# Optimization experiments

Measured on AMD Instinct MI355X. Metric: run time of the kernel, lower is better.

The kernel has to match this reference:

```python
import jax, jax.numpy as jnp
import numpy as np

N, E, D, L1 = 100000, 1600000, 128, 64


def setup_inputs() -> dict:
    key = jax.random.key(0)
    ks = jax.random.split(key, 8)
    return {
        "x": jax.random.normal(ks[0], (N, D), dtype=jnp.float32),
        "edge_index": jax.random.randint(ks[1], (2, E), 0, N, dtype=jnp.int64),
        "W1_rel": jax.random.normal(ks[2], (L1, D), dtype=jnp.float32) * (1.0 / np.sqrt(D)),
        "b1": jax.random.normal(ks[3], (L1,), dtype=jnp.float32) * 0.01,
        "W1_root": jax.random.normal(ks[4], (L1, D), dtype=jnp.float32) * (1.0 / np.sqrt(D)),
        "W2_rel": jax.random.normal(ks[5], (1, L1), dtype=jnp.float32) * (1.0 / np.sqrt(L1)),
        "b2": jax.random.normal(ks[6], (1,), dtype=jnp.float32) * 0.01,
        "W2_root": jax.random.normal(ks[7], (1, L1), dtype=jnp.float32) * (1.0 / np.sqrt(L1)),
    }


def _graph_conv(h, src, dst, W_rel, b, W_root, n):
    # PyG GraphConv: lin_rel(sum_{j in N(i)} h_j) + lin_root(h_i)
    agg = jax.ops.segment_sum(h[src], dst, num_segments=n)  # [N, d_in]
    return agg @ W_rel.T + b + h @ W_root.T


def reference(x, edge_index, W1_rel, b1, W1_root, W2_rel, b2, W2_root):
    src, dst = edge_index[0], edge_index[1]
    n = x.shape[0]
    h = _graph_conv(x, src, dst, W1_rel, b1, W1_root, n)        # [N, L1]
    h = jax.nn.leaky_relu(h, negative_slope=0.2)                # dropout is identity in eval
    gate = _graph_conv(h, src, dst, W2_rel, b2, W2_root, n)     # [N, 1]
    gate = jax.nn.softmax(gate, axis=0)                         # softmax over nodes
    out = gate.T @ x                                            # [1, D]
    return out
```

## Files before the change

kernel.cpp:

```cpp
#include <hip/hip_runtime.h>
#include <cstdint>

#define DD 128
#define LL 64
#define PSTRIDE 64
#define NCHUNK 256
#define BPAD 784

typedef short short8 __attribute__((ext_vector_type(8)));
typedef float f32x4 __attribute__((ext_vector_type(4)));

static __device__ __forceinline__ unsigned short f2bf(float f) {
    unsigned u = __float_as_uint(f);
    unsigned r = (u + 0x7FFFu + ((u >> 16) & 1u)) >> 16;
    return (unsigned short)r;
}
static __device__ __forceinline__ float bf2f(unsigned short h) {
    return __uint_as_float(((unsigned)h) << 16);
}
static __device__ __forceinline__ uint4 pack8(float4 lo, float4 hi) {
    uint4 u;
    u.x = (unsigned)f2bf(lo.x) | ((unsigned)f2bf(lo.y) << 16);
    u.y = (unsigned)f2bf(lo.z) | ((unsigned)f2bf(lo.w) << 16);
    u.z = (unsigned)f2bf(hi.x) | ((unsigned)f2bf(hi.y) << 16);
    u.w = (unsigned)f2bf(hi.z) | ((unsigned)f2bf(hi.w) << 16);
    return u;
}

__global__ __launch_bounds__(256) void k1_scat(const float* __restrict__ x,
        const float* __restrict__ Wrel, const float* __restrict__ Wroot,
        const int* __restrict__ dst, int* __restrict__ cm,
        unsigned short* __restrict__ yb, unsigned short* __restrict__ zb,
        int n, int E)
{
    __shared__ __align__(16) unsigned short xa[64 * 128];
    int tid = threadIdx.x;
    if (blockIdx.x < NCHUNK) {
        int* hist = (int*)xa;
        int c = blockIdx.x;
        for (int i = tid; i < BPAD; i += 256) hist[i] = 0;
        __syncthreads();
        int CH = (E + NCHUNK - 1) / NCHUNK;
        int base = c * CH, end = base + CH; if (end > E) end = E;
        for (int e = base + tid; e < end; e += 256)
            atomicAdd(&hist[dst[e] >> 7], 1);
        __syncthreads();
        for (int i = tid; i < BPAD; i += 256) cm[c * BPAD + i] = hist[i];
        return;
    }
    int nbase = (blockIdx.x - NCHUNK) * 64;

    {
        int r = tid & 63, cb = (tid >> 6) * 4;
        int node = nbase + r; if (node >= n) node = n - 1;
        const float4* xp = (const float4*)(x + (size_t)node * DD + cb * 8);
        #pragma unroll
        for (int c = 0; c < 4; ++c) {
            float4 lo = xp[c * 2], hi = xp[c * 2 + 1];
            int slot = (cb + c + r) & 15;
            *(uint4*)&xa[r * 128 + slot * 8] = pack8(lo, hi);
        }
    }
    __syncthreads();

    int lane = tid & 63;
    int w = __builtin_amdgcn_readfirstlane(tid >> 6);
    int lr = lane & 15, lk = lane >> 4;
    const float* __restrict__ Wsel = (w < 2) ? Wrel : Wroot;
    int rbase = (w & 1) * 32;

    f32x4 acc[4][2];
    #pragma unroll
    for (int tr = 0; tr < 4; ++tr)
        #pragma unroll
        for (int tc = 0; tc < 2; ++tc)
            acc[tr][tc] = (f32x4){0.f, 0.f, 0.f, 0.f};

    #pragma unroll
    for (int kk = 0; kk < 4; ++kk) {
        int c = kk * 4 + lk;
        short8 bfrag[2];
        #pragma unroll
        for (int tc = 0; tc < 2; ++tc) {
            const float* wp = Wsel + (size_t)(rbase + tc * 16 + lr) * DD + kk * 32 + lk * 8;
            float4 lo = *(const float4*)wp;
            float4 hi = *(const float4*)(wp + 4);
            uint4 u = pack8(lo, hi);
            bfrag[tc] = *(short8*)&u;
        }
        #pragma unroll
        for (int tr = 0; tr < 4; ++tr) {
            int arow = tr * 16 + lr;
            short8 afrag = *(const short8*)&xa[arow * 128 + ((c + arow) & 15) * 8];
            acc[tr][0] = __builtin_amdgcn_mfma_f32_16x16x32_bf16(afrag, bfrag[0], acc[tr][0], 0, 0, 0);
            acc[tr][1] = __builtin_amdgcn_mfma_f32_16x16x32_bf16(afrag, bfrag[1], acc[tr][1], 0, 0, 0);
        }
    }

    __syncthreads();
    unsigned short* ob = xa;
    #pragma unroll
    for (int tr = 0; tr < 4; ++tr) {
        #pragma unroll
        for (int tc = 0; tc < 2; ++tc) {
            int col = w * 32 + tc * 16 + lr;
            int cg = col >> 4, ci = col & 15;
            #pragma unroll
            for (int r = 0; r < 4; ++r) {
                int row = tr * 16 + lk * 4 + r;
                ob[row * 128 + ((cg ^ (row & 7)) << 4) + ci] = f2bf(acc[tr][tc][r]);
            }
        }
    }
    __syncthreads();

    {
        int row = tid >> 2, part = tid & 3;
        int node = nbase + row;
        if (node < n) {
            int by = row * 128 + ((part ^ (row & 7)) << 4);
            uint4 a0 = *(uint4*)&ob[by];
            uint4 a1 = *(uint4*)&ob[by + 8];
            *(uint4*)(yb + (size_t)node * LL + part * 16) = a0;
            *(uint4*)(yb + (size_t)node * LL + part * 16 + 8) = a1;
            int bz = row * 128 + (((part + 4) ^ (row & 7)) << 4);
            uint4 b0 = *(uint4*)&ob[bz];
            uint4 b1 = *(uint4*)&ob[bz + 8];
            *(uint4*)(zb + (size_t)node * LL + part * 16) = b0;
            *(uint4*)(zb + (size_t)node * LL + part * 16 + 8) = b1;
        }
    }
}

__global__ __launch_bounds__(1024) void kB(int* __restrict__ cm, int* __restrict__ bbase, int E) {
    __shared__ int sc[1024];
    int b = threadIdx.x;
    int tot = 0;
    if (b < BPAD)
        for (int c = 0; c < NCHUNK; ++c) tot += cm[c * BPAD + b];
    sc[b] = tot;
    __syncthreads();
    for (int off = 1; off < 1024; off <<= 1) {
        int add = (b >= off) ? sc[b - off] : 0;
        __syncthreads();
        sc[b] += add;
        __syncthreads();
    }
    int excl = sc[b] - tot;
    if (b < BPAD) bbase[b] = excl;
    if (b == 1023) bbase[BPAD] = sc[b];
    if (b < BPAD) {
        int run = excl;
        for (int c = 0; c < NCHUNK; ++c) {
            int v = cm[c * BPAD + b];
            cm[c * BPAD + b] = run;
            run += v;
        }
    }
}

__global__ __launch_bounds__(256) void kC(const int* __restrict__ src, const int* __restrict__ dst,
        const int* __restrict__ cm, int* __restrict__ sorted, int E)
{
    __shared__ int run[BPAD];
    int c = blockIdx.x;
    for (int i = threadIdx.x; i < BPAD; i += 256) run[i] = cm[c * BPAD + i];
    __syncthreads();
    int CH = (E + NCHUNK - 1) / NCHUNK;
    int base = c * CH, end = base + CH; if (end > E) end = E;
    for (int e = base + threadIdx.x; e < end; e += 256) {
        int d = dst[e];
        int pos = atomicAdd(&run[d >> 7], 1);
        sorted[pos] = ((d & 127) << 17) | src[e];
    }
}

__global__ __launch_bounds__(256) void kD(const int* __restrict__ sorted, const int* __restrict__ bbase,
        int* __restrict__ cnt, int* __restrict__ csr_pad, int n)
{
    __shared__ int hist[128];
    int b = blockIdx.x;
    int lo = bbase[b], hi = bbase[b + 1];
    for (int i = threadIdx.x; i < 128; i += 256) hist[i] = 0;
    __syncthreads();
    for (int e = lo + threadIdx.x; e < hi; e += 256) {
        int v = sorted[e];
        int loc = v >> 17;
        int pos = atomicAdd(&hist[loc], 1);
        if (pos < PSTRIDE)
            csr_pad[(size_t)(b * 128 + loc) * PSTRIDE + pos] = v & 0x1FFFF;
    }
    __syncthreads();
    for (int i = threadIdx.x; i < 128; i += 256) {
        int node = b * 128 + i;
        if (node < n) cnt[node] = hist[i];
    }
}

__global__ __launch_bounds__(256) void k3_agg(const unsigned short* __restrict__ yb, const unsigned short* __restrict__ zb,
        const int* __restrict__ cnt, const int* __restrict__ csr_pad,
        const float* __restrict__ b1, const float* __restrict__ w2rel, const float* __restrict__ w2root,
        float* __restrict__ s, float* __restrict__ t, int n)
{
    int wave = threadIdx.x >> 6, lane = threadIdx.x & 63;
    int i = blockIdx.x * 4 + wave;
    if (i >= n) return;
    int deg = cnt[i]; if (deg > PSTRIDE) deg = PSTRIDE;
    const int* cp = csr_pad + (size_t)i * PSTRIDE;
    int c2 = lane & 31, half = lane >> 5;
    float ax = 0.f, ay = 0.f;
    int k = 0;
    for (; k + 4 <= deg; k += 4) {
        int sA0 = cp[k], sB0 = cp[k + 1], sA1 = cp[k + 2], sB1 = cp[k + 3];
        int r0 = half ? sB0 : sA0;
        int r1 = half ? sB1 : sA1;
        unsigned u0 = *(const unsigned*)(yb + (size_t)r0 * LL + c2 * 2);
        unsigned u1 = *(const unsigned*)(yb + (size_t)r1 * LL + c2 * 2);
        ax += bf2f((unsigned short)u0) + bf2f((unsigned short)u1);
        ay += bf2f((unsigned short)(u0 >> 16)) + bf2f((unsigned short)(u1 >> 16));
    }
    if (k + 2 <= deg) {
        int rA = cp[k], rB = cp[k + 1];
        int r = half ? rB : rA;
        unsigned u = *(const unsigned*)(yb + (size_t)r * LL + c2 * 2);
        ax += bf2f((unsigned short)u);
        ay += bf2f((unsigned short)(u >> 16));
        k += 2;
    }
    if (k < deg && !half) {
        int r = cp[k];
        unsigned u = *(const unsigned*)(yb + (size_t)r * LL + c2 * 2);
        ax += bf2f((unsigned short)u);
        ay += bf2f((unsigned short)(u >> 16));
    }
    ax += __shfl_xor(ax, 32, 64);
    ay += __shfl_xor(ay, 32, 64);

    unsigned uz = *(const unsigned*)(zb + (size_t)i * LL + c2 * 2);
    float hx = ax + bf2f((unsigned short)uz) + b1[c2 * 2];
    float hy = ay + bf2f((unsigned short)(uz >> 16)) + b1[c2 * 2 + 1];
    hx = hx > 0.f ? hx : 0.2f * hx;
    hy = hy > 0.f ? hy : 0.2f * hy;
    float sv = hx * w2rel[c2 * 2] + hy * w2rel[c2 * 2 + 1];
    float tv = hx * w2root[c2 * 2] + hy * w2root[c2 * 2 + 1];
    #pragma unroll
    for (int o = 16; o >= 1; o >>= 1) {
        sv += __shfl_xor(sv, o, 64);
        tv += __shfl_xor(tv, o, 64);
    }
    if (lane == 0) { s[i] = sv; t[i] = tv; }
}

static __device__ __forceinline__ void smcomb(float& m, float& Z, float m2, float Z2) {
    float M = fmaxf(m, m2);
    Z = Z * expf(m - M) + Z2 * expf(m2 - M);
    m = M;
}

__global__ __launch_bounds__(256) void k5_gate(const float* __restrict__ s, const float* __restrict__ t,
        const int* __restrict__ cnt, const int* __restrict__ csr_pad, const float* __restrict__ b2,
        float* __restrict__ g, float2* __restrict__ pairs, int n)
{
    __shared__ float sm[256], sz[256];
    int i = blockIdx.x * 256 + threadIdx.x;
    float m = -3.402823466e38f, Z = 0.f;
    if (i < n) {
        float acc = b2[0] + t[i];
        int deg = cnt[i]; if (deg > PSTRIDE) deg = PSTRIDE;
        const int* cp = csr_pad + (size_t)i * PSTRIDE;
        int e = 0;
        for (; e + 4 <= deg; e += 4)
            acc += (s[cp[e]] + s[cp[e + 1]]) + (s[cp[e + 2]] + s[cp[e + 3]]);
        for (; e < deg; ++e) acc += s[cp[e]];
        g[i] = acc;
        m = acc; Z = 1.f;
    }
    sm[threadIdx.x] = m; sz[threadIdx.x] = Z;
    __syncthreads();
    for (int off = 128; off > 0; off >>= 1) {
        if (threadIdx.x < off) {
            float mm = sm[threadIdx.x], ZZ = sz[threadIdx.x];
            smcomb(mm, ZZ, sm[threadIdx.x + off], sz[threadIdx.x + off]);
            sm[threadIdx.x] = mm; sz[threadIdx.x] = ZZ;
        }
        __syncthreads();
    }
    if (threadIdx.x == 0) pairs[blockIdx.x] = make_float2(sm[0], sz[0]);
}

__global__ __launch_bounds__(256) void k6b(const float2* __restrict__ pairs, float* __restrict__ scalars, int nb) {
    __shared__ float sm[256], sz[256];
    float m = -3.402823466e38f, Z = 0.f;
    for (int j = threadIdx.x; j < nb; j += 256) {
        float2 p = pairs[j];
        smcomb(m, Z, p.x, p.y);
    }
    sm[threadIdx.x] = m; sz[threadIdx.x] = Z;
    __syncthreads();
    for (int off = 128; off > 0; off >>= 1) {
        if (threadIdx.x < off) {
            float mm = sm[threadIdx.x], ZZ = sz[threadIdx.x];
            smcomb(mm, ZZ, sm[threadIdx.x + off], sz[threadIdx.x + off]);
            sm[threadIdx.x] = mm; sz[threadIdx.x] = ZZ;
        }
        __syncthreads();
    }
    if (threadIdx.x == 0) { scalars[0] = sm[0]; scalars[1] = sz[0]; }
}

__global__ __launch_bounds__(256) void k6_out(const float* __restrict__ x, const float* __restrict__ g,
        const float* __restrict__ scalars, float* __restrict__ out, int n)
{
    __shared__ float acc_s[4][DD];
    int wave = threadIdx.x >> 6, lane = threadIdx.x & 63;
    float m = scalars[0];
    float invZ = 1.0f / scalars[1];
    float a0 = 0.f, a1 = 0.f;
    int gw = blockIdx.x * 4 + wave;
    int nw = gridDim.x * 4;
    for (int i = gw; i < n; i += nw) {
        float w = expf(g[i] - m) * invZ;
        a0 += w * x[(size_t)i * DD + lane];
        a1 += w * x[(size_t)i * DD + 64 + lane];
    }
    acc_s[wave][lane] = a0;
    acc_s[wave][lane + 64] = a1;
    __syncthreads();
    if (wave == 0) {
        float v0 = acc_s[0][lane] + acc_s[1][lane] + acc_s[2][lane] + acc_s[3][lane];
        float v1 = acc_s[0][lane + 64] + acc_s[1][lane + 64] + acc_s[2][lane + 64] + acc_s[3][lane + 64];
        atomicAdd(&out[lane], v0);
        atomicAdd(&out[lane + 64], v1);
    }
}

extern "C" void kernel_launch(void* const* d_in, const int* in_sizes, int n_in,
                              void* d_out, int out_size, void* d_ws, size_t ws_size,
                              hipStream_t stream)
{
    const float* x      = (const float*)d_in[0];
    const int*   eidx   = (const int*)d_in[1];
    const float* W1rel  = (const float*)d_in[2];
    const float* b1     = (const float*)d_in[3];
    const float* W1root = (const float*)d_in[4];
    const float* W2rel  = (const float*)d_in[5];
    const float* b2     = (const float*)d_in[6];
    const float* W2root = (const float*)d_in[7];
    float* out = (float*)d_out;

    int n = in_sizes[0] / DD;
    int E = in_sizes[1] / 2;
    const int* src = eidx;
    const int* dstp = eidx + E;
    int NBK = (n + 127) >> 7;

    char* ws = (char*)d_ws;
    size_t off = 0;
    auto alloc = [&](size_t bytes) -> char* {
        char* p = ws + off;
        off = (off + bytes + 255) & ~(size_t)255;
        return p;
    };
    unsigned short* yb = (unsigned short*)alloc((size_t)n * LL * 2);
    unsigned short* zb = (unsigned short*)alloc((size_t)n * LL * 2);
    int*   cnt     = (int*)  alloc((size_t)n * 4);
    int*   csr_pad = (int*)  alloc((size_t)NBK * 128 * PSTRIDE * 4);
    int*   cm      = (int*)  alloc((size_t)NCHUNK * BPAD * 4);
    int*   bbase   = (int*)  alloc((size_t)(BPAD + 1) * 4);
    int*   sorted  = (int*)  alloc((size_t)E * 4);
    float* s       = (float*)alloc((size_t)n * 4);
    float* t       = (float*)alloc((size_t)n * 4);
    float* g       = (float*)alloc((size_t)n * 4);
    int ngate = (n + 255) / 256;
    float2* pairs  = (float2*)alloc((size_t)ngate * 8);
    float* scalars = (float*)alloc(2 * 4);
    (void)ws_size; (void)n_in;

    hipMemsetAsync(d_out, 0, (size_t)out_size * 4, stream);

    int nblk1 = (n + 63) / 64;
    k1_scat<<<NCHUNK + nblk1, 256, 0, stream>>>(x, W1rel, W1root, dstp, cm, yb, zb, n, E);
    kB<<<1, 1024, 0, stream>>>(cm, bbase, E);
    kC<<<NCHUNK, 256, 0, stream>>>(src, dstp, cm, sorted, E);
    kD<<<NBK, 256, 0, stream>>>(sorted, bbase, cnt, csr_pad, n);
    k3_agg<<<(n + 3) / 4, 256, 0, stream>>>(yb, zb, cnt, csr_pad, b1, W2rel, W2root, s, t, n);
    k5_gate<<<ngate, 256, 0, stream>>>(s, t, cnt, csr_pad, b2, g, pairs, n);
    k6b<<<1, 256, 0, stream>>>(pairs, scalars, ngate);
    k6_out<<<512, 256, 0, stream>>>(x, g, scalars, out, n);
}
```

Before: 203.8 us.

## Split bucket scan, coalesce x staging, unroll aggregation gather deeper

The single-block scan kernel, which walked the whole chunk-by-bucket count matrix twice with 784 threads, becomes two kernels. One does per-bucket running sums across 4 blocks, and a tiny kernel scans the bucket totals, with kC adding the bucket base when it loads its offsets. The x staging load in k1 now assigns four threads per row, so neighbouring threads read contiguous memory. The k3 gather loop is unrolled from 4 to 8 edges per iteration to keep more loads in flight, and the bf16 unpack of the high half uses a mask instead of a shift. This adds one extra kernel launch in exchange.

```diff
diff --git a/kernel.cpp b/kernel.cpp
--- a/kernel.cpp
+++ b/kernel.cpp
@@ -15,8 +15,11 @@
     unsigned r = (u + 0x7FFFu + ((u >> 16) & 1u)) >> 16;
     return (unsigned short)r;
 }
-static __device__ __forceinline__ float bf2f(unsigned short h) {
-    return __uint_as_float(((unsigned)h) << 16);
+static __device__ __forceinline__ float bflo(unsigned u) {
+    return __uint_as_float(u << 16);
+}
+static __device__ __forceinline__ float bfhi(unsigned u) {
+    return __uint_as_float(u & 0xFFFF0000u);
 }
 static __device__ __forceinline__ uint4 pack8(float4 lo, float4 hi) {
     uint4 u;
@@ -51,12 +54,12 @@
     int nbase = (blockIdx.x - NCHUNK) * 64;
 
     {
-        int r = tid & 63, cb = (tid >> 6) * 4;
+        int r = tid >> 2, cb = (tid & 3) * 4;
         int node = nbase + r; if (node >= n) node = n - 1;
-        const float4* xp = (const float4*)(x + (size_t)node * DD + cb * 8);
+        const float4* xp = (const float4*)(x + (size_t)node * DD);
         #pragma unroll
         for (int c = 0; c < 4; ++c) {
-            float4 lo = xp[c * 2], hi = xp[c * 2 + 1];
+            float4 lo = xp[(cb + c) * 2], hi = xp[(cb + c) * 2 + 1];
             int slot = (cb + c + r) & 15;
             *(uint4*)&xa[r * 128 + slot * 8] = pack8(lo, hi);
         }
@@ -132,13 +135,23 @@
     }
 }
 
-__global__ __launch_bounds__(1024) void kB(int* __restrict__ cm, int* __restrict__ bbase, int E) {
+__global__ __launch_bounds__(256) void kB1(int* __restrict__ cm, int* __restrict__ btot) {
+    int b = blockIdx.x * 256 + threadIdx.x;
+    if (b >= BPAD) return;
+    int run = 0;
+    for (int c = 0; c < NCHUNK; ++c) {
+        int v = cm[c * BPAD + b];
+        cm[c * BPAD + b] = run;
+        run += v;
+    }
+    btot[b] = run;
+}
+
+__global__ __launch_bounds__(1024) void kB2(const int* __restrict__ btot, int* __restrict__ bbase) {
     __shared__ int sc[1024];
     int b = threadIdx.x;
-    int tot = 0;
-    if (b < BPAD)
-        for (int c = 0; c < NCHUNK; ++c) tot += cm[c * BPAD + b];
-    sc[b] = tot;
+    int v = (b < BPAD) ? btot[b] : 0;
+    sc[b] = v;
     __syncthreads();
     for (int off = 1; off < 1024; off <<= 1) {
         int add = (b >= off) ? sc[b - off] : 0;
@@ -146,25 +159,16 @@
         sc[b] += add;
         __syncthreads();
     }
-    int excl = sc[b] - tot;
-    if (b < BPAD) bbase[b] = excl;
+    if (b < BPAD) bbase[b] = sc[b] - v;
     if (b == 1023) bbase[BPAD] = sc[b];
-    if (b < BPAD) {
-        int run = excl;
-        for (int c = 0; c < NCHUNK; ++c) {
-            int v = cm[c * BPAD + b];
-            cm[c * BPAD + b] = run;
-            run += v;
-        }
-    }
 }
 
 __global__ __launch_bounds__(256) void kC(const int* __restrict__ src, const int* __restrict__ dst,
-        const int* __restrict__ cm, int* __restrict__ sorted, int E)
+        const int* __restrict__ cm, const int* __restrict__ bbase, int* __restrict__ sorted, int E)
 {
     __shared__ int run[BPAD];
     int c = blockIdx.x;
-    for (int i = threadIdx.x; i < BPAD; i += 256) run[i] = cm[c * BPAD + i];
+    for (int i = threadIdx.x; i < BPAD; i += 256) run[i] = cm[c * BPAD + i] + bbase[i];
     __syncthreads();
     int CH = (E + NCHUNK - 1) / NCHUNK;
     int base = c * CH, end = base + CH; if (end > E) end = E;
@@ -210,35 +214,35 @@
     int c2 = lane & 31, half = lane >> 5;
     float ax = 0.f, ay = 0.f;
     int k = 0;
-    for (; k + 4 <= deg; k += 4) {
-        int sA0 = cp[k], sB0 = cp[k + 1], sA1 = cp[k + 2], sB1 = cp[k + 3];
-        int r0 = half ? sB0 : sA0;
-        int r1 = half ? sB1 : sA1;
+    for (; k + 8 <= deg; k += 8) {
+        int r0 = half ? cp[k + 1] : cp[k + 0];
+        int r1 = half ? cp[k + 3] : cp[k + 2];
+        int r2 = half ? cp[k + 5] : cp[k + 4];
+        int r3 = half ? cp[k + 7] : cp[k + 6];
         unsigned u0 = *(const unsigned*)(yb + (size_t)r0 * LL + c2 * 2);
         unsigned u1 = *(const unsigned*)(yb + (size_t)r1 * LL + c2 * 2);
-        ax += bf2f((unsigned short)u0) + bf2f((unsigned short)u1);
-        ay += bf2f((unsigned short)(u0 >> 16)) + bf2f((unsigned short)(u1 >> 16));
-    }
-    if (k + 2 <= deg) {
-        int rA = cp[k], rB = cp[k + 1];
-        int r = half ? rB : rA;
+        unsigned u2 = *(const unsigned*)(yb + (size_t)r2 * LL + c2 * 2);
+        unsigned u3 = *(const unsigned*)(yb + (size_t)r3 * LL + c2 * 2);
+        ax += (bflo(u0) + bflo(u1)) + (bflo(u2) + bflo(u3));
+        ay += (bfhi(u0) + bfhi(u1)) + (bfhi(u2) + bfhi(u3));
+    }
+    for (; k + 2 <= deg; k += 2) {
+        int r = half ? cp[k + 1] : cp[k];
         unsigned u = *(const unsigned*)(yb + (size_t)r * LL + c2 * 2);
-        ax += bf2f((unsigned short)u);
-        ay += bf2f((unsigned short)(u >> 16));
-        k += 2;
+        ax += bflo(u);
+        ay += bfhi(u);
     }
     if (k < deg && !half) {
-        int r = cp[k];
-        unsigned u = *(const unsigned*)(yb + (size_t)r * LL + c2 * 2);
-        ax += bf2f((unsigned short)u);
-        ay += bf2f((unsigned short)(u >> 16));
+        unsigned u = *(const unsigned*)(yb + (size_t)cp[k] * LL + c2 * 2);
+        ax += bflo(u);
+        ay += bfhi(u);
     }
     ax += __shfl_xor(ax, 32, 64);
     ay += __shfl_xor(ay, 32, 64);
 
     unsigned uz = *(const unsigned*)(zb + (size_t)i * LL + c2 * 2);
-    float hx = ax + bf2f((unsigned short)uz) + b1[c2 * 2];
-    float hy = ay + bf2f((unsigned short)(uz >> 16)) + b1[c2 * 2 + 1];
+    float hx = ax + bflo(uz) + b1[c2 * 2];
+    float hy = ay + bfhi(uz) + b1[c2 * 2 + 1];
     hx = hx > 0.f ? hx : 0.2f * hx;
     hy = hy > 0.f ? hy : 0.2f * hy;
     float sv = hx * w2rel[c2 * 2] + hy * w2rel[c2 * 2 + 1];
@@ -366,6 +370,7 @@
     int*   cnt     = (int*)  alloc((size_t)n * 4);
     int*   csr_pad = (int*)  alloc((size_t)NBK * 128 * PSTRIDE * 4);
     int*   cm      = (int*)  alloc((size_t)NCHUNK * BPAD * 4);
+    int*   btot    = (int*)  alloc((size_t)BPAD * 4);
     int*   bbase   = (int*)  alloc((size_t)(BPAD + 1) * 4);
     int*   sorted  = (int*)  alloc((size_t)E * 4);
     float* s       = (float*)alloc((size_t)n * 4);
@@ -380,8 +385,9 @@
 
     int nblk1 = (n + 63) / 64;
     k1_scat<<<NCHUNK + nblk1, 256, 0, stream>>>(x, W1rel, W1root, dstp, cm, yb, zb, n, E);
-    kB<<<1, 1024, 0, stream>>>(cm, bbase, E);
-    kC<<<NCHUNK, 256, 0, stream>>>(src, dstp, cm, sorted, E);
+    kB1<<<(BPAD + 255) / 256, 256, 0, stream>>>(cm, btot);
+    kB2<<<1, 1024, 0, stream>>>(btot, bbase);
+    kC<<<NCHUNK, 256, 0, stream>>>(src, dstp, cm, bbase, sorted, E);
     kD<<<NBK, 256, 0, stream>>>(sorted, bbase, cnt, csr_pad, n);
     k3_agg<<<(n + 3) / 4, 256, 0, stream>>>(yb, zb, cnt, csr_pad, b1, W2rel, W2root, s, t, n);
     k5_gate<<<ngate, 256, 0, stream>>>(s, t, cnt, csr_pad, b2, g, pairs, n);
```

Result: faster. 184.6 us (-9.4%).
